# Performance work log

Measured on AMD Instinct MI355X. Metric: run time of the kernel, lower is better.

The kernel has to match this reference:

```python
import jax, jax.numpy as jnp
import numpy as np

B, S, D = 8, 1024, 2048
H, HD = 16, 128          # n_heads, head_dim (H*HD == D)
ROPE = 64                # rotary dims per head (front slice)
MAXB, MAXS = 10, 1024    # kv-cache buffer sizes (hardcoded in module)
START_POS = 0


def _apply_rope(x, cos_half, sin_half):
    # x: (BH, S, ROPE); cos/sin_half: (S, ROPE//2) -> tiled to (S, ROPE)
    cos_full = jnp.concatenate([cos_half, cos_half], axis=-1)
    sin_full = jnp.concatenate([sin_half, sin_half], axis=-1)
    half = x.shape[-1] // 2
    x1, x2 = x[..., :half], x[..., half:]
    rotated = jnp.concatenate([-x2, x1], axis=-1)
    return x * cos_full + rotated * sin_full


def setup_inputs() -> dict:
    key = jax.random.key(0)
    ks = jax.random.split(key, 6)
    sc = 0.02
    x = jax.random.normal(ks[0], (B, S, D), dtype=jnp.float32)
    wq = jax.random.normal(ks[1], (D, D), dtype=jnp.float32) * sc
    wk = jax.random.normal(ks[2], (D, D), dtype=jnp.float32) * sc
    wv = jax.random.normal(ks[3], (D, D), dtype=jnp.float32) * sc
    wo = jax.random.normal(ks[4], (D, D), dtype=jnp.float32) * sc
    bq = jnp.zeros((D,), jnp.float32)
    bk = jnp.zeros((D,), jnp.float32)
    bv = jnp.zeros((D,), jnp.float32)
    bo = jnp.zeros((D,), jnp.float32)
    # RoPE tables (HF "half" layout): angles over positions
    half = ROPE // 2
    inv_freq = 1.0 / (10000.0 ** (jnp.arange(half, dtype=jnp.float32) / half))
    ang = jnp.arange(S, dtype=jnp.float32)[:, None] * inv_freq[None, :]  # (S, half)
    cos_half = jnp.cos(ang)
    sin_half = jnp.sin(ang)
    mask = jnp.zeros((S, S), jnp.float32)  # additive mask, (seq, end_pos)
    cache_k = jnp.zeros((MAXB, MAXS, H * HD), jnp.float32)
    cache_v = jnp.zeros((MAXB, MAXS, H * HD), jnp.float32)
    return {
        "x": x, "wq": wq, "bq": bq, "wk": wk, "bk": bk, "wv": wv, "bv": bv,
        "wo": wo, "bo": bo, "cos_half": cos_half, "sin_half": sin_half,
        "mask": mask, "cache_k": cache_k, "cache_v": cache_v,
        "start_pos": START_POS,
    }


def reference(x, wq, bq, wk, bk, wv, bv, wo, bo, cos_half, sin_half, mask,
              cache_k, cache_v, start_pos):
    b, s, _ = x.shape
    end_pos = start_pos + s
    # QKV projections (torch Linear: y = x @ W.T + b)
    q = (x @ wq.T + bq).reshape(b, s, H, HD)
    k = (x @ wk.T + bk).reshape(b, s, H, HD)
    v = (x @ wv.T + bv).reshape(b, s, H, HD)
    # Partial RoPE on the first ROPE dims of each head
    q_head = q[..., :ROPE].transpose(0, 2, 1, 3).reshape(b * H, s, ROPE)
    k_head = k[..., :ROPE].transpose(0, 2, 1, 3).reshape(b * H, s, ROPE)
    q_head = _apply_rope(q_head, cos_half, sin_half)
    k_head = _apply_rope(k_head, cos_half, sin_half)
    q_head = q_head.reshape(b, H, s, ROPE).transpose(0, 2, 1, 3)
    k_head = k_head.reshape(b, H, s, ROPE).transpose(0, 2, 1, 3)
    q = jnp.concatenate([q_head, q[..., ROPE:]], axis=-1)
    k = jnp.concatenate([k_head, k[..., ROPE:]], axis=-1)
    # KV-cache write then read (start_pos is a static python int)
    cache_k = jax.lax.dynamic_update_slice(cache_k, k.reshape(b, s, H * HD), (0, start_pos, 0))
    cache_v = jax.lax.dynamic_update_slice(cache_v, v.reshape(b, s, H * HD), (0, start_pos, 0))
    k_cached = cache_k[:b, :end_pos].reshape(b, end_pos, H, HD)
    v_cached = cache_v[:b, :end_pos].reshape(b, end_pos, H, HD)
    # Unnormalized attention: no softmax, no scaling
    scores = jnp.einsum('bshd,bthd->bsht', q, k_cached)  # (B,S,H,T)
    scores = scores + mask[:, None, :]                   # (S,1,T) broadcast
    a_sum = jnp.einsum('bsht,bthd->bshd', scores, v_cached)
    out = a_sum.reshape(b, s, H * HD) @ wo.T + bo
    return out
```

## Files before the change

### kernel.cpp

```cpp
#include <hip/hip_runtime.h>
#include <stdint.h>

#define B_ 8
#define S_ 1024
#define D_ 2048
#define H_ 16
#define HD_ 128
#define NROW 8192
#define NQKV 6144

typedef __bf16 bf16;
typedef bf16  bf16x8 __attribute__((ext_vector_type(8)));
typedef bf16  bf16x4 __attribute__((ext_vector_type(4)));
typedef float f32x4  __attribute__((ext_vector_type(4)));

#define AS1 __attribute__((address_space(1)))
#define AS3 __attribute__((address_space(3)))

__device__ __forceinline__ void gl_lds16(const bf16* g, bf16* l) {
  __builtin_amdgcn_global_load_lds((AS1 void*)g, (AS3 void*)l, 16, 0, 0);
}

__global__ __launch_bounds__(256) void f2b4(const float* __restrict__ in,
                                            bf16* __restrict__ out, int n4) {
  int i = blockIdx.x * 256 + threadIdx.x;
  if (i >= n4) return;
  float4 v = reinterpret_cast<const float4*>(in)[i];
  bf16x4 o;
  o.x = (bf16)v.x; o.y = (bf16)v.y; o.z = (bf16)v.z; o.w = (bf16)v.w;
  reinterpret_cast<bf16x4*>(out)[i] = o;
}

__global__ void packb(const float* __restrict__ a, const float* __restrict__ b,
                      const float* __restrict__ c, float* __restrict__ o) {
  int i = blockIdx.x * 256 + threadIdx.x;
  if (i >= NQKV) return;
  o[i] = (i < 2048) ? a[i] : (i < 4096 ? b[i - 2048] : c[i - 4096]);
}

#define READ_A4(QA, KS, Ab)                                                   \
  _Pragma("unroll") for (int mi = 0; mi < 4; mi++)                            \
    af[mi] = *reinterpret_cast<const bf16x8*>(                                \
        (Ab) + aoff + ((((QA)*4 + mi)*2) + (KS))*512);

#define READ_B4(KS, Bb)                                                       \
  _Pragma("unroll") for (int ni = 0; ni < 4; ni++)                            \
    bfr[ni] = *reinterpret_cast<const bf16x8*>(                               \
        (Bb) + boff + ((ni*2) + (KS))*512);

#define MFMA16(QA)                                                            \
  _Pragma("unroll") for (int mi = 0; mi < 4; mi++)                            \
  _Pragma("unroll") for (int ni = 0; ni < 4; ni++)                            \
    acc[(QA)*4 + mi][ni] = __builtin_amdgcn_mfma_f32_16x16x32_bf16(           \
        af[mi], bfr[ni], acc[(QA)*4 + mi][ni], 0, 0, 0);

#define STAGE_H0(An, Bn, koff)                                                \
  gl_lds16(agA + (koff),           (An) + wid*1024);                          \
  gl_lds16(agA + 128*la + (koff),  (An) + (wid + 8)*1024);                    \
  gl_lds16(agB + (koff),           (Bn) + wid*1024);                          \
  gl_lds16(agB + 128*lb + (koff),  (Bn) + (wid + 8)*1024);

#define STAGE_H1(An, Bn, koff)                                                \
  gl_lds16(agA + (koff) + 32,          (An) + wid*1024 + 512);                \
  gl_lds16(agA + 128*la + (koff) + 32, (An) + (wid + 8)*1024 + 512);          \
  gl_lds16(agB + (koff) + 32,          (Bn) + wid*1024 + 512);                \
  gl_lds16(agB + 128*lb + (koff) + 32, (Bn) + (wid + 8)*1024 + 512);

template <typename CT, bool BIAS, bool ACCUM>
__global__ __launch_bounds__(512, 2) void gemm256(const bf16* __restrict__ A,
                                                  const bf16* __restrict__ Bm,
                                                  const float* __restrict__ bias,
                                                  CT* __restrict__ C,
                                                  int M, int N, int K,
                                                  long la, long lb, long lc,
                                                  long za, long zb, long zc) {
  extern __shared__ __align__(16) bf16 lds[];
  const int z = blockIdx.z;
  A  += (long)z * za;
  Bm += (long)z * zb;
  C  += (long)z * zc;
  const int tid  = threadIdx.x;
  const int wid  = tid >> 6;
  const int lane = tid & 63;
  const int wm0 = (wid >> 2) * 128;
  const int wn0 = (wid & 3) * 64;
  const int m0 = blockIdx.y * 256, n0 = blockIdx.x * 256;

  const int rr = lane >> 2;
  const int cc = ((lane & 3) * 8) ^ ((rr & 8) << 1);
  const bf16* agA = A  + (long)(m0 + wid * 16 + rr) * la + cc;
  const bf16* agB = Bm + (long)(n0 + wid * 16 + rr) * lb + cc;

  const int swz  = ((lane >> 4) * 8) ^ ((lane & 8) << 1);
  const int aoff = (wm0 >> 4) * 1024 + (lane & 15) * 32 + swz;
  const int boff = (wn0 >> 4) * 1024 + (lane & 15) * 32 + swz;

  f32x4 acc[8][4] = {};
  const int NT = K >> 6;

  { bf16* An = lds; bf16* Bn = lds + 16384;
    STAGE_H0(An, Bn, 0); STAGE_H1(An, Bn, 0); }

  for (int t = 0; t < NT; ++t) {
    const bf16* Ab = lds + (t & 1) * 32768;
    const bf16* Bb = Ab + 16384;
    bf16* An = lds + ((t & 1) ^ 1) * 32768;
    bf16* Bn = An + 16384;
    const long kn = (long)(t + 1) * 64;
    const bool pf = (t + 1) < NT;
    bf16x8 af[4], bfr[4];

    asm volatile("s_waitcnt vmcnt(4)" ::: "memory");
    __builtin_amdgcn_s_barrier();
    READ_A4(0, 0, Ab); READ_B4(0, Bb);
    if (pf) { STAGE_H0(An, Bn, kn); }
    asm volatile("s_waitcnt lgkmcnt(0)" ::: "memory");
    __builtin_amdgcn_sched_barrier(0);
    __builtin_amdgcn_s_setprio(1); MFMA16(0); __builtin_amdgcn_s_setprio(0);

    READ_A4(1, 0, Ab);
    asm volatile("s_waitcnt lgkmcnt(0)" ::: "memory");
    __builtin_amdgcn_sched_barrier(0);
    __builtin_amdgcn_s_setprio(1); MFMA16(1); __builtin_amdgcn_s_setprio(0);

    if (pf) asm volatile("s_waitcnt vmcnt(4)" ::: "memory");
    else    asm volatile("s_waitcnt vmcnt(0)" ::: "memory");
    __builtin_amdgcn_s_barrier();
    READ_A4(0, 1, Ab); READ_B4(1, Bb);
    if (pf) { STAGE_H1(An, Bn, kn); }
    asm volatile("s_waitcnt lgkmcnt(0)" ::: "memory");
    __builtin_amdgcn_sched_barrier(0);
    __builtin_amdgcn_s_setprio(1); MFMA16(0); __builtin_amdgcn_s_setprio(0);

    READ_A4(1, 1, Ab);
    asm volatile("s_waitcnt lgkmcnt(0)" ::: "memory");
    __builtin_amdgcn_sched_barrier(0);
    __builtin_amdgcn_s_setprio(1); MFMA16(1); __builtin_amdgcn_s_setprio(0);
  }

#pragma unroll
  for (int mi = 0; mi < 8; mi++) {
#pragma unroll
    for (int ni = 0; ni < 4; ni++) {
      const int col = n0 + wn0 + ni * 16 + (lane & 15);
      float bv = 0.0f;
      if constexpr (BIAS) bv = bias[col];
      const long base = (long)(m0 + wm0 + mi * 16 + (lane >> 4) * 4) * lc + col;
#pragma unroll
      for (int r = 0; r < 4; r++) {
        float v = acc[mi][ni][r] + bv;
        if constexpr (ACCUM) v += (float)C[base + (long)r * lc];
        C[base + (long)r * lc] = (CT)v;
      }
    }
  }
}

template <typename CT, bool BIAS, bool ACCUM>
__global__ __launch_bounds__(256) void gemm_bt(const bf16* __restrict__ A,
                                               const bf16* __restrict__ Bm,
                                               const float* __restrict__ bias,
                                               CT* __restrict__ C,
                                               int M, int N, int K,
                                               long la, long lb, long lc,
                                               long za, long zb, long zc) {
  __shared__ __align__(16) bf16 As[128 * 32];
  __shared__ __align__(16) bf16 Bs[128 * 32];
  const int z = blockIdx.z;
  A  += (long)z * za;
  Bm += (long)z * zb;
  C  += (long)z * zc;
  const int tid = threadIdx.x;
  const int w = tid >> 6, l = tid & 63;
  const int wm = (w & 1) * 64, wn = (w >> 1) * 64;
  const int m0 = blockIdx.y * 128, n0 = blockIdx.x * 128;
  const int lr = l & 15, lk = (l >> 4) * 8;
  const int er = (l >> 4) * 4;

  const bf16* ag = A  + (long)(m0 + (tid >> 2)) * la + (tid & 3) * 8;
  const bf16* bg = Bm + (long)(n0 + (tid >> 2)) * lb + (tid & 3) * 8;
  bf16* al = As + (w * 16) * 32;
  bf16* bl = Bs + (w * 16) * 32;

  f32x4 acc[4][4] = {};

  for (int k0 = 0; k0 < K; k0 += 32) {
    gl_lds16(ag + k0,            al);
    gl_lds16(ag + 64 * la + k0,  al + 64 * 32);
    gl_lds16(bg + k0,            bl);
    gl_lds16(bg + 64 * lb + k0,  bl + 64 * 32);
    __syncthreads();
    bf16x8 afr[4], bfr[4];
#pragma unroll
    for (int mi = 0; mi < 4; mi++)
      afr[mi] = *reinterpret_cast<const bf16x8*>(As + (wm + mi * 16 + lr) * 32 + lk);
#pragma unroll
    for (int ni = 0; ni < 4; ni++)
      bfr[ni] = *reinterpret_cast<const bf16x8*>(Bs + (wn + ni * 16 + lr) * 32 + lk);
#pragma unroll
    for (int mi = 0; mi < 4; mi++)
#pragma unroll
      for (int ni = 0; ni < 4; ni++)
        acc[mi][ni] = __builtin_amdgcn_mfma_f32_16x16x32_bf16(afr[mi], bfr[ni], acc[mi][ni], 0, 0, 0);
    __syncthreads();
  }

#pragma unroll
  for (int mi = 0; mi < 4; mi++) {
#pragma unroll
    for (int ni = 0; ni < 4; ni++) {
      const int col = n0 + wn + ni * 16 + lr;
      float bv = 0.0f;
      if constexpr (BIAS) bv = bias[col];
      const long base = (long)(m0 + wm + mi * 16 + er) * lc + col;
#pragma unroll
      for (int r = 0; r < 4; r++) {
        float v = acc[mi][ni][r] + bv;
        if constexpr (ACCUM) v += (float)C[base + (long)r * lc];
        C[base + (long)r * lc] = (CT)v;
      }
    }
  }
}

__global__ __launch_bounds__(256) void rope_qk(bf16* __restrict__ QKV,
                                               const float* __restrict__ ch,
                                               const float* __restrict__ sh) {
  int idx = blockIdx.x * 256 + threadIdx.x;
  if (idx >= NROW * H_ * 2 * 32) return;
  int hd = idx & 31;
  int qk = (idx >> 5) & 1;
  int h  = (idx >> 6) & 15;
  int row = idx >> 10;
  int s = row & (S_ - 1);
  long base = (long)row * NQKV + qk * 2048 + h * HD_ + hd;
  float a  = (float)QKV[base];
  float b2 = (float)QKV[base + 32];
  float c = ch[s * 32 + hd], sn = sh[s * 32 + hd];
  QKV[base]      = (bf16)(a * c - b2 * sn);
  QKV[base + 32] = (bf16)(b2 * c + a * sn);
}

__global__ __launch_bounds__(256) void kvtrans(const bf16* __restrict__ QKV,
                                               bf16* __restrict__ Kt,
                                               bf16* __restrict__ Vt) {
  __shared__ unsigned short T[128 * 130];
  const int bid = blockIdx.x;
  const int tb = bid & 7, bh = (bid >> 3) & 127, kv = bid >> 10;
  const int b = bh >> 4, h = bh & 15;
  const int tid = threadIdx.x;
  const bf16* src = QKV + (long)(b * S_ + tb * 128) * NQKV + 2048 + kv * 2048 + h * HD_;
#pragma unroll
  for (int it = 0; it < 8; it++) {
    int chunk = it * 256 + tid;
    int r = chunk >> 4, hc = (chunk & 15) * 8;
    bf16x8 v = *reinterpret_cast<const bf16x8*>(src + (long)r * NQKV + hc);
    union { bf16x8 v8; unsigned short u[8]; } u8; u8.v8 = v;
#pragma unroll
    for (int j = 0; j < 8; j++) T[r * 130 + hc + j] = u8.u[j];
  }
  __syncthreads();
  bf16* dst = (kv ? Vt : Kt) + (long)bh * HD_ * S_ + tb * 128;
#pragma unroll
  for (int it = 0; it < 8; it++) {
    int chunk = it * 256 + tid;
    int hd = chunk >> 4, tc = (chunk & 15) * 8;
    union { bf16x8 v8; unsigned short u[8]; } u8;
#pragma unroll
    for (int j = 0; j < 8; j++) u8.u[j] = T[(tc + j) * 130 + hd];
    *reinterpret_cast<bf16x8*>(dst + (long)hd * S_ + tc) = u8.v8;
  }
}

__global__ __launch_bounds__(256) void qw2_gemm(const bf16* __restrict__ QKV,
                                                const bf16* __restrict__ W2,
                                                bf16* __restrict__ Ob) {
  __shared__ __align__(16) bf16 As[128 * 32];
  __shared__ __align__(16) bf16 Bs[128 * 32];
  const int z = blockIdx.z;
  const int b = z >> 4, h = z & 15;
  const int m0 = blockIdx.y * 128;
  const int tid = threadIdx.x;
  const int w = tid >> 6, l = tid & 63;
  const int wm = (w & 1) * 64, wn = (w >> 1) * 64;
  const int lr = l & 15, lk = (l >> 4) * 8;
  const int er = (l >> 4) * 4;

  const bf16* ag = QKV + (long)(b * S_ + m0 + (tid >> 2)) * NQKV + h * HD_ + (tid & 3) * 8;
  const bf16* bg = W2 + (long)z * (HD_ * HD_) + (tid >> 2) * HD_ + (tid & 3) * 8;
  bf16* al = As + (w * 16) * 32;
  bf16* bl = Bs + (w * 16) * 32;

  f32x4 acc[4][4] = {};

#pragma unroll
  for (int k0 = 0; k0 < HD_; k0 += 32) {
    gl_lds16(ag + k0,                   al);
    gl_lds16(ag + (long)64 * NQKV + k0, al + 64 * 32);
    gl_lds16(bg + k0,                   bl);
    gl_lds16(bg + 64 * HD_ + k0,        bl + 64 * 32);
    __syncthreads();
    bf16x8 afr[4], bfr[4];
#pragma unroll
    for (int mi = 0; mi < 4; mi++)
      afr[mi] = *reinterpret_cast<const bf16x8*>(As + (wm + mi * 16 + lr) * 32 + lk);
#pragma unroll
    for (int ni = 0; ni < 4; ni++)
      bfr[ni] = *reinterpret_cast<const bf16x8*>(Bs + (wn + ni * 16 + lr) * 32 + lk);
#pragma unroll
    for (int mi = 0; mi < 4; mi++)
#pragma unroll
      for (int ni = 0; ni < 4; ni++)
        acc[mi][ni] = __builtin_amdgcn_mfma_f32_16x16x32_bf16(afr[mi], bfr[ni], acc[mi][ni], 0, 0, 0);
    __syncthreads();
  }

#pragma unroll
  for (int mi = 0; mi < 4; mi++) {
#pragma unroll
    for (int ni = 0; ni < 4; ni++) {
      const int col = h * HD_ + wn + ni * 16 + lr;
#pragma unroll
      for (int r = 0; r < 4; r++) {
        const int sl = m0 + wm + mi * 16 + er + r;
        const long idx = (long)(b * S_ + sl) * D_ + col;
        Ob[idx] = (bf16)((float)Ob[idx] + acc[mi][ni][r]);
      }
    }
  }
}

extern "C" void kernel_launch(void* const* d_in, const int* in_sizes, int n_in,
                              void* d_out, int out_size, void* d_ws, size_t ws_size,
                              hipStream_t stream) {
  const float* x   = (const float*)d_in[0];
  const float* wq  = (const float*)d_in[1];
  const float* bq  = (const float*)d_in[2];
  const float* wk  = (const float*)d_in[3];
  const float* bk  = (const float*)d_in[4];
  const float* wv  = (const float*)d_in[5];
  const float* bv  = (const float*)d_in[6];
  const float* wo  = (const float*)d_in[7];
  const float* bo  = (const float*)d_in[8];
  const float* ch  = (const float*)d_in[9];
  const float* sh  = (const float*)d_in[10];
  const float* mask = (const float*)d_in[11];
  float* out = (float*)d_out;

  hipFuncSetAttribute(reinterpret_cast<const void*>(&gemm256<bf16, true, false>),
                      hipFuncAttributeMaxDynamicSharedMemorySize, 131072);
  hipFuncSetAttribute(reinterpret_cast<const void*>(&gemm256<bf16, false, false>),
                      hipFuncAttributeMaxDynamicSharedMemorySize, 131072);
  hipFuncSetAttribute(reinterpret_cast<const void*>(&gemm256<float, true, false>),
                      hipFuncAttributeMaxDynamicSharedMemorySize, 131072);

  char* ws = (char*)d_ws;
  bf16*  QKV   = (bf16*)(ws);
  bf16*  Vt    = (bf16*)(ws + 100663296);
  bf16*  Kt    = (bf16*)(ws + 134217728);
  bf16*  wob   = (bf16*)(ws + 167772160);
  float* bqkv  = (float*)(ws + 176160768);
  bf16*  maskb = (bf16*)(ws + 176185344);
  bf16*  W2    = (bf16*)(ws + 178282496);
  bf16*  Ob    = (bf16*)(ws + 182476800);
  bf16*  xb    = (bf16*)(ws + 216031232);
  bf16*  wqkvb = (bf16*)(ws + 249585664);

  f2b4<<<16384, 256, 0, stream>>>(x, xb, 4194304);
  f2b4<<<4096, 256, 0, stream>>>(wq, wqkvb,           1048576);
  f2b4<<<4096, 256, 0, stream>>>(wk, wqkvb + 4194304, 1048576);
  f2b4<<<4096, 256, 0, stream>>>(wv, wqkvb + 8388608, 1048576);
  f2b4<<<4096, 256, 0, stream>>>(wo, wob, 1048576);
  f2b4<<<1024, 256, 0, stream>>>(mask, maskb, 262144);
  packb<<<24, 256, 0, stream>>>(bq, bk, bv, bqkv);

  gemm256<bf16, true, false><<<dim3(24, 32, 1), 512, 131072, stream>>>(
      xb, wqkvb, bqkv, QKV, NROW, NQKV, D_,
      (long)D_, (long)D_, (long)NQKV, 0L, 0L, 0L);

  rope_qk<<<32768, 256, 0, stream>>>(QKV, ch, sh);
  kvtrans<<<2048, 256, 0, stream>>>(QKV, Kt, Vt);

  gemm_bt<bf16, false, false><<<dim3(1, 1, 128), 256, 0, stream>>>(
      Vt, Kt, nullptr, W2, HD_, HD_, S_,
      (long)S_, (long)S_, (long)HD_,
      (long)(HD_ * S_), (long)(HD_ * S_), (long)(HD_ * HD_));

  gemm256<bf16, false, false><<<dim3(8, 4, 8), 512, 131072, stream>>>(
      maskb, Vt, nullptr, Ob, S_, D_, S_,
      (long)S_, (long)S_, (long)D_,
      0L, (long)(D_ * S_), (long)(S_ * D_));

  qw2_gemm<<<dim3(1, 8, 128), 256, 0, stream>>>(QKV, W2, Ob);

  gemm256<float, true, false><<<dim3(8, 32, 1), 512, 131072, stream>>>(
      Ob, wob, bo, out, NROW, D_, D_,
      (long)D_, (long)D_, (long)D_, 0L, 0L, 0L);
}
```

Baseline: 632.9 us.

## Fuse input conversion kernels and deepen GEMM prefetch by a half-tile

The seven fp32-to-bf16 conversion and bias-pack launches are merged into one prep kernel, which removes launch overhead and tail gaps between them. The gemm256 main loop now issues its global-to-LDS loads one half-stage further ahead: it stages the second half of tile t+1 and the first half of tile t+2 while computing tile t, and waits on vmcnt(8) instead of vmcnt(4). This is meant to hide more memory latency. The cost is more outstanding loads and tighter reuse of the LDS buffers, and it relies on the barrier ordering to avoid overwriting data that is still being read.

```diff
diff --git a/kernel.cpp b/kernel.cpp
--- a/kernel.cpp
+++ b/kernel.cpp
@@ -21,21 +21,38 @@
   __builtin_amdgcn_global_load_lds((AS1 void*)g, (AS3 void*)l, 16, 0, 0);
 }
 
-__global__ __launch_bounds__(256) void f2b4(const float* __restrict__ in,
-                                            bf16* __restrict__ out, int n4) {
-  int i = blockIdx.x * 256 + threadIdx.x;
-  if (i >= n4) return;
-  float4 v = reinterpret_cast<const float4*>(in)[i];
-  bf16x4 o;
-  o.x = (bf16)v.x; o.y = (bf16)v.y; o.z = (bf16)v.z; o.w = (bf16)v.w;
-  reinterpret_cast<bf16x4*>(out)[i] = o;
-}
-
-__global__ void packb(const float* __restrict__ a, const float* __restrict__ b,
-                      const float* __restrict__ c, float* __restrict__ o) {
-  int i = blockIdx.x * 256 + threadIdx.x;
-  if (i >= NQKV) return;
-  o[i] = (i < 2048) ? a[i] : (i < 4096 ? b[i - 2048] : c[i - 4096]);
+__global__ __launch_bounds__(256) void prep(const float* __restrict__ x,
+                                            const float* __restrict__ wq,
+                                            const float* __restrict__ wk,
+                                            const float* __restrict__ wv,
+                                            const float* __restrict__ wo,
+                                            const float* __restrict__ mask,
+                                            const float* __restrict__ bq,
+                                            const float* __restrict__ bk,
+                                            const float* __restrict__ bv,
+                                            bf16* __restrict__ xb,
+                                            bf16* __restrict__ wqkvb,
+                                            bf16* __restrict__ wob,
+                                            bf16* __restrict__ maskb,
+                                            float* __restrict__ bqkv) {
+  long i = (long)blockIdx.x * 256 + threadIdx.x;
+  if (i < 8650752) {
+    const float* src; bf16* dst; long j;
+    if (i < 4194304)      { src = x;    dst = xb;              j = i; }
+    else if (i < 5242880) { src = wq;   dst = wqkvb;           j = i - 4194304; }
+    else if (i < 6291456) { src = wk;   dst = wqkvb + 4194304; j = i - 5242880; }
+    else if (i < 7340032) { src = wv;   dst = wqkvb + 8388608; j = i - 6291456; }
+    else if (i < 8388608) { src = wo;   dst = wob;             j = i - 7340032; }
+    else                  { src = mask; dst = maskb;           j = i - 8388608; }
+    float4 v = reinterpret_cast<const float4*>(src)[j];
+    bf16x4 o;
+    o.x = (bf16)v.x; o.y = (bf16)v.y; o.z = (bf16)v.z; o.w = (bf16)v.w;
+    reinterpret_cast<bf16x4*>(dst)[j] = o;
+  } else {
+    long e = (i - 8650752) * 4;
+    const float* s = (e < 2048) ? bq + e : (e < 4096 ? bk + (e - 2048) : bv + (e - 4096));
+    *reinterpret_cast<float4*>(bqkv + e) = *reinterpret_cast<const float4*>(s);
+  }
 }
 
 #define READ_A4(QA, KS, Ab)                                                   \
@@ -100,20 +117,25 @@
 
   { bf16* An = lds; bf16* Bn = lds + 16384;
     STAGE_H0(An, Bn, 0); STAGE_H1(An, Bn, 0); }
+  { bf16* An = lds + 32768; bf16* Bn = lds + 49152;
+    STAGE_H0(An, Bn, 64); }
 
   for (int t = 0; t < NT; ++t) {
     const bf16* Ab = lds + (t & 1) * 32768;
     const bf16* Bb = Ab + 16384;
-    bf16* An = lds + ((t & 1) ^ 1) * 32768;
-    bf16* Bn = An + 16384;
-    const long kn = (long)(t + 1) * 64;
-    const bool pf = (t + 1) < NT;
+    bf16* An1 = lds + ((t & 1) ^ 1) * 32768;
+    bf16* Bn1 = An1 + 16384;
+    bf16* An2 = lds + (t & 1) * 32768;
+    bf16* Bn2 = An2 + 16384;
+    const bool pf1 = (t + 1) < NT;
+    const bool pf2 = (t + 2) < NT;
     bf16x8 af[4], bfr[4];
 
-    asm volatile("s_waitcnt vmcnt(4)" ::: "memory");
+    if (pf1) asm volatile("s_waitcnt vmcnt(8)" ::: "memory");
+    else     asm volatile("s_waitcnt vmcnt(4)" ::: "memory");
     __builtin_amdgcn_s_barrier();
     READ_A4(0, 0, Ab); READ_B4(0, Bb);
-    if (pf) { STAGE_H0(An, Bn, kn); }
+    if (pf1) { STAGE_H1(An1, Bn1, (long)(t + 1) * 64); }
     asm volatile("s_waitcnt lgkmcnt(0)" ::: "memory");
     __builtin_amdgcn_sched_barrier(0);
     __builtin_amdgcn_s_setprio(1); MFMA16(0); __builtin_amdgcn_s_setprio(0);
@@ -123,11 +145,11 @@
     __builtin_amdgcn_sched_barrier(0);
     __builtin_amdgcn_s_setprio(1); MFMA16(1); __builtin_amdgcn_s_setprio(0);
 
-    if (pf) asm volatile("s_waitcnt vmcnt(4)" ::: "memory");
-    else    asm volatile("s_waitcnt vmcnt(0)" ::: "memory");
+    if (pf1) asm volatile("s_waitcnt vmcnt(8)" ::: "memory");
+    else     asm volatile("s_waitcnt vmcnt(0)" ::: "memory");
     __builtin_amdgcn_s_barrier();
     READ_A4(0, 1, Ab); READ_B4(1, Bb);
-    if (pf) { STAGE_H1(An, Bn, kn); }
+    if (pf2) { STAGE_H0(An2, Bn2, (long)(t + 2) * 64); }
     asm volatile("s_waitcnt lgkmcnt(0)" ::: "memory");
     __builtin_amdgcn_sched_barrier(0);
     __builtin_amdgcn_s_setprio(1); MFMA16(0); __builtin_amdgcn_s_setprio(0);
@@ -366,13 +388,8 @@
   bf16*  xb    = (bf16*)(ws + 216031232);
   bf16*  wqkvb = (bf16*)(ws + 249585664);
 
-  f2b4<<<16384, 256, 0, stream>>>(x, xb, 4194304);
-  f2b4<<<4096, 256, 0, stream>>>(wq, wqkvb,           1048576);
-  f2b4<<<4096, 256, 0, stream>>>(wk, wqkvb + 4194304, 1048576);
-  f2b4<<<4096, 256, 0, stream>>>(wv, wqkvb + 8388608, 1048576);
-  f2b4<<<4096, 256, 0, stream>>>(wo, wob, 1048576);
-  f2b4<<<1024, 256, 0, stream>>>(mask, maskb, 262144);
-  packb<<<24, 256, 0, stream>>>(bq, bk, bv, bqkv);
+  prep<<<33798, 256, 0, stream>>>(x, wq, wk, wv, wo, mask, bq, bk, bv,
+                                  xb, wqkvb, wob, maskb, bqkv);
 
   gemm256<bf16, true, false><<<dim3(24, 32, 1), 512, 131072, stream>>>(
       xb, wqkvb, bqkv, QKV, NROW, NQKV, D_,
```

New measurement: 630.3 us. Within noise of the previous version (-0.4%).
